# Optimization experiments

Measured on AMD Instinct MI355X. Metric: run time of the kernel, lower is better.

Reference implementation:

```python
import jax, jax.numpy as jnp
import numpy as np

D_MODEL = 1024
NHEAD = 16
DFF = 4096
EPS = 1e-5


def layer_norm(x, g, b, eps=EPS):
    mu = jnp.mean(x, axis=-1, keepdims=True)
    var = jnp.var(x, axis=-1, keepdims=True)
    return (x - mu) * jax.lax.rsqrt(var + eps) * g + b


def setup_inputs() -> dict:
    key = jax.random.key(0)
    ks = jax.random.split(key, 8)
    S, N, E = 1024, 8, D_MODEL
    s = 0.02
    return {
        "src": jax.random.normal(ks[0], (S, N, E), dtype=jnp.float32),
        "in_proj_w": jax.random.normal(ks[1], (3 * E, E), dtype=jnp.float32) * s,
        "in_proj_b": jnp.zeros((3 * E,), dtype=jnp.float32),
        "out_w": jax.random.normal(ks[2], (E, E), dtype=jnp.float32) * s,
        "out_b": jnp.zeros((E,), dtype=jnp.float32),
        "w1": jax.random.normal(ks[3], (DFF, E), dtype=jnp.float32) * s,
        "b1": jnp.zeros((DFF,), dtype=jnp.float32),
        "w2": jax.random.normal(ks[4], (E, DFF), dtype=jnp.float32) * s,
        "b2": jnp.zeros((E,), dtype=jnp.float32),
        "ln1_g": jnp.ones((E,), dtype=jnp.float32),
        "ln1_b": jnp.zeros((E,), dtype=jnp.float32),
        "ln2_g": jnp.ones((E,), dtype=jnp.float32),
        "ln2_b": jnp.zeros((E,), dtype=jnp.float32),
    }


def reference(src, in_proj_w, in_proj_b, out_w, out_b, w1, b1, w2, b2,
              ln1_g, ln1_b, ln2_g, ln2_b):
    S, N, E = src.shape
    H = NHEAD
    D = E // H
    scale = 1.0 / jnp.sqrt(jnp.asarray(D, src.dtype))

    # fused QKV projection (PyTorch in_proj): [S,N,3E]
    qkv = src @ in_proj_w.T + in_proj_b
    q, k, v = jnp.split(qkv, 3, axis=-1)
    # [S,N,E] -> [N,H,S,D]
    def to_heads(t):
        return t.reshape(S, N, H, D).transpose(1, 2, 0, 3)
    q, k, v = to_heads(q), to_heads(k), to_heads(v)

    # explicit QK^T / softmax / AV (need_weights=True path)
    scores = jnp.einsum('nhsd,nhtd->nhst', q * scale, k)  # [N,H,S,S]
    attn = jax.nn.softmax(scores, axis=-1)
    ctx = jnp.einsum('nhst,nhtd->nhsd', attn, v)          # [N,H,S,D]
    ctx = ctx.transpose(2, 0, 1, 3).reshape(S, N, E)
    attn_out = ctx @ out_w.T + out_b

    # avg over heads (PyTorch default average_attn_weights=True): [N,S,S]
    attn_weights = jnp.mean(attn, axis=1)

    # post-norm residual structure (norm_first=False), dropout=0 (eval)
    x = layer_norm(src + attn_out, ln1_g, ln1_b)
    ff = jax.nn.relu(x @ w1.T + b1) @ w2.T + b2
    x = layer_norm(x + ff, ln2_g, ln2_b)
    return x, attn_weights
```

## Files before the change

kernel.cpp:

```cpp
#include <hip/hip_runtime.h>

typedef __attribute__((ext_vector_type(4))) float f32x4;
typedef __attribute__((ext_vector_type(8))) short short8;
typedef __attribute__((ext_vector_type(4))) unsigned short u16x4;

#define MFMA(a,b,c) __builtin_amdgcn_mfma_f32_16x16x32_bf16(a,b,c,0,0,0)

__device__ __forceinline__ unsigned short f2bf(float x){
    union { float f; unsigned int u; } c; c.f = x;
    unsigned int u = c.u;
    unsigned int r = (u + 0x7fffu + ((u >> 16) & 1u)) >> 16;
    return (unsigned short)r;
}
__device__ __forceinline__ float bf2f(unsigned short h){
    union { unsigned int u; float f; } c; c.u = ((unsigned int)h) << 16;
    return c.f;
}

__device__ __forceinline__ void load16_lds(const unsigned short* g, unsigned short* l){
    __builtin_amdgcn_global_load_lds(
        (const __attribute__((address_space(1))) unsigned int*)g,
        (__attribute__((address_space(3))) unsigned int*)l, 16, 0, 0);
}

#define SWZ_IDX(row, col, stride) \
    ((row)*(stride) + (((((col) >> 3) ^ ((row) & 7)) << 3) | ((col) & 7)))

__global__ __launch_bounds__(256) void cast_f32_bf16(const float* __restrict__ in,
                                                     unsigned short* __restrict__ out, int n4){
    int i = blockIdx.x * 256 + threadIdx.x;
    if (i < n4){
        const float4* in4 = (const float4*)in;
        float4 v = in4[i];
        u16x4 o;
        o[0] = f2bf(v.x); o[1] = f2bf(v.y); o[2] = f2bf(v.z); o[3] = f2bf(v.w);
        ((u16x4*)out)[i] = o;
    }
}

template<int OUT_BF16, int RELU>
__global__ __launch_bounds__(256) void gemm_bt(const unsigned short* __restrict__ A,
                                               const unsigned short* __restrict__ W,
                                               const float* __restrict__ bias,
                                               void* __restrict__ Cout,
                                               int M, int N, int K)
{
    __shared__ unsigned short As[128*32];
    __shared__ unsigned short Bs[128*32];
    const int tid  = threadIdx.x;
    const int wave = tid >> 6, lane = tid & 63;
    const int bm = blockIdx.x, bn = blockIdx.y;
    const int wr = wave >> 1, wc = wave & 1;
    const int lr = lane & 15, lg = lane >> 4;

    f32x4 acc[4][4] = {};

    const size_t arow0 = (size_t)bm * 128;
    const size_t brow0 = (size_t)bn * 128;

    for (int k0 = 0; k0 < K; k0 += 32){
        __syncthreads();
        #pragma unroll
        for (int i = 0; i < 2; ++i){
            int c = i*256 + wave*64 + lane;
            int row = c >> 2, cc = c & 3;
            load16_lds(A + (arow0 + row)*K + k0 + cc*8, As + (size_t)(i*256 + wave*64)*8);
            load16_lds(W + (brow0 + row)*K + k0 + cc*8, Bs + (size_t)(i*256 + wave*64)*8);
        }
        __syncthreads();
        short8 af[4], bfr[4];
        #pragma unroll
        for (int mi = 0; mi < 4; ++mi)
            af[mi] = *(const short8*)(As + (wr*64 + mi*16 + lr)*32 + lg*8);
        #pragma unroll
        for (int ni = 0; ni < 4; ++ni)
            bfr[ni] = *(const short8*)(Bs + (wc*64 + ni*16 + lr)*32 + lg*8);
        #pragma unroll
        for (int mi = 0; mi < 4; ++mi)
            #pragma unroll
            for (int ni = 0; ni < 4; ++ni)
                acc[mi][ni] = MFMA(af[mi], bfr[ni], acc[mi][ni]);
    }

    #pragma unroll
    for (int ni = 0; ni < 4; ++ni){
        int col = bn*128 + wc*64 + ni*16 + lr;
        float bv = bias ? bias[col] : 0.0f;
        #pragma unroll
        for (int mi = 0; mi < 4; ++mi){
            int row0 = bm*128 + wr*64 + mi*16 + lg*4;
            #pragma unroll
            for (int j = 0; j < 4; ++j){
                float v = acc[mi][ni][j] + bv;
                if (RELU) v = v > 0.0f ? v : 0.0f;
                if (OUT_BF16) ((unsigned short*)Cout)[(size_t)(row0+j)*N + col] = f2bf(v);
                else          ((float*)Cout)[(size_t)(row0+j)*N + col] = v;
            }
        }
    }
}

__global__ __launch_bounds__(256) void transpose_v(const unsigned short* __restrict__ qkv,
                                                   unsigned short* __restrict__ vt)
{
    __shared__ unsigned short tile[64][80];
    const int tt = blockIdx.x, h = blockIdx.y, n = blockIdx.z;
    const int tid = threadIdx.x;
    #pragma unroll
    for (int i = 0; i < 2; ++i){
        int c = i*256 + tid;
        int row = c >> 3, cc = c & 7;
        short8 v = *(const short8*)(qkv + ((size_t)(tt*64+row)*8 + n)*3072 + 2048 + h*64 + cc*8);
        *(short8*)&tile[row][cc*8] = v;
    }
    __syncthreads();
    #pragma unroll
    for (int i = 0; i < 2; ++i){
        int c = i*256 + tid;
        int drow = c >> 3, cc = c & 7;
        short8 o;
        #pragma unroll
        for (int j = 0; j < 8; ++j) o[j] = tile[cc*8+j][drow];
        *(short8*)(vt + ((size_t)(n*16+h)*64 + drow)*1024 + tt*64 + cc*8) = o;
    }
}

__global__ __launch_bounds__(256) void attn_fused(const unsigned short* __restrict__ qkv,
                                                  const unsigned short* __restrict__ vt,
                                                  float2* __restrict__ stats,
                                                  unsigned short* __restrict__ ctx)
{
    __shared__ unsigned short qs[32*64];
    __shared__ unsigned short kt[64*64];
    __shared__ unsigned short vtile[64*64];
    __shared__ unsigned short pt[32*64];
    __shared__ float wl[4][32];
    __shared__ float rowinv[32];
    const int qb = blockIdx.x, h = blockIdx.y, n = blockIdx.z;
    const int tid = threadIdx.x;
    const int wave = tid >> 6, lane = tid & 63;
    const int lr = lane & 15, lg = lane >> 4;
    const int s0 = qb * 32;
    const float scale = 0.125f;

    {
        int row = tid >> 3, cc = tid & 7;
        *(short8*)(qs + SWZ_IDX(row, cc*8, 64)) =
            *(const short8*)(qkv + ((size_t)(s0+row)*8 + n)*3072 + h*64 + cc*8);
    }

    float lsum[2][4] = {};
    f32x4 av[2] = {};

    for (int tt = 0; tt < 16; ++tt){
        __syncthreads();
        #pragma unroll
        for (int i = 0; i < 2; ++i){
            int c = i*256 + wave*64 + lane;
            int row = c >> 3, sl = (c & 7) ^ (row & 7);
            load16_lds(qkv + ((size_t)(tt*64+row)*8 + n)*3072 + 1024 + h*64 + sl*8,
                       kt + (size_t)(i*256 + wave*64)*8);
            load16_lds(vt + ((size_t)(n*16+h)*64 + row)*1024 + tt*64 + sl*8,
                       vtile + (size_t)(i*256 + wave*64)*8);
        }
        __syncthreads();

        f32x4 acc[2] = {};
        #pragma unroll
        for (int kk = 0; kk < 2; ++kk){
            short8 b  = *(const short8*)(kt + SWZ_IDX(wave*16 + lr, kk*32 + lg*8, 64));
            short8 a0 = *(const short8*)(qs + SWZ_IDX(lr,          kk*32 + lg*8, 64));
            short8 a1 = *(const short8*)(qs + SWZ_IDX(16 + lr,     kk*32 + lg*8, 64));
            acc[0] = MFMA(a0, b, acc[0]);
            acc[1] = MFMA(a1, b, acc[1]);
        }
        #pragma unroll
        for (int mi = 0; mi < 2; ++mi)
            #pragma unroll
            for (int j = 0; j < 4; ++j){
                float p = __expf(fminf(acc[mi][j] * scale, 80.0f));
                lsum[mi][j] += p;
                pt[SWZ_IDX(mi*16 + lg*4 + j, wave*16 + lr, 64)] = f2bf(p);
            }
        __syncthreads();

        #pragma unroll
        for (int kk = 0; kk < 2; ++kk){
            short8 b  = *(const short8*)(vtile + SWZ_IDX(wave*16 + lr, kk*32 + lg*8, 64));
            short8 a0 = *(const short8*)(pt + SWZ_IDX(lr,      kk*32 + lg*8, 64));
            short8 a1 = *(const short8*)(pt + SWZ_IDX(16 + lr, kk*32 + lg*8, 64));
            av[0] = MFMA(a0, b, av[0]);
            av[1] = MFMA(a1, b, av[1]);
        }
    }

    #pragma unroll
    for (int mi = 0; mi < 2; ++mi)
        #pragma unroll
        for (int j = 0; j < 4; ++j){
            float v = lsum[mi][j];
            v += __shfl_xor(v, 1);
            v += __shfl_xor(v, 2);
            v += __shfl_xor(v, 4);
            v += __shfl_xor(v, 8);
            if (lr == 0) wl[wave][mi*16 + lg*4 + j] = v;
        }
    __syncthreads();
    if (tid < 32){
        float l = wl[0][tid] + wl[1][tid] + wl[2][tid] + wl[3][tid];
        float inv = 1.0f / l;
        rowinv[tid] = inv;
        stats[((size_t)(n*16+h)*1024) + s0 + tid] = make_float2(0.0f, inv * 0.0625f);
    }
    __syncthreads();

    #pragma unroll
    for (int mi = 0; mi < 2; ++mi)
        #pragma unroll
        for (int j = 0; j < 4; ++j){
            int lrow = mi*16 + lg*4 + j;
            int srow = s0 + lrow;
            int d = wave*16 + lr;
            ctx[((size_t)srow*8 + n)*1024 + h*64 + d] = f2bf(av[mi][j] * rowinv[lrow]);
        }
}

__global__ __launch_bounds__(256) void attn_mean(const unsigned short* __restrict__ qkv,
                                                 const float2* __restrict__ stats,
                                                 float* __restrict__ attw)
{
    __shared__ unsigned short qs[16*1024];
    __shared__ unsigned short kv[2][4][16*128];
    __shared__ float2 smL[16][16];
    const int qb = blockIdx.x, n = blockIdx.y;
    const int tid = threadIdx.x;
    const int wave = tid >> 6, lane = tid & 63;
    const int lr = lane & 15, lg = lane >> 4;
    const int s0 = qb * 16;
    const float scale = 0.125f;

    {
        int head = tid >> 4, row = tid & 15;
        smL[head][row] = stats[((size_t)(n*16+head)*1024) + s0 + row];
    }
    #pragma unroll
    for (int i = 0; i < 8; ++i){
        int c = i*256 + tid;
        int row = c >> 7, cc = c & 127;
        *(short8*)(qs + SWZ_IDX(row, cc*8, 1024)) =
            *(const short8*)(qkv + ((size_t)(s0+row)*8 + n)*3072 + cc*8);
    }

    unsigned short* kvw = &kv[0][wave][0];
    const int KVBUF = 4*16*128;

    auto stage = [&](int buf, int tt, int g){
        #pragma unroll
        for (int i = 0; i < 4; ++i){
            int c2 = i*64 + lane;
            int rw = c2 >> 4;
            int sd = c2 & 15;
            int sl = sd ^ (rw & 7);
            int trow = tt*64 + wave*16 + rw;
            load16_lds(qkv + ((size_t)trow*8 + n)*3072 + 1024 + g*128 + sl*8,
                       kvw + buf*KVBUF + i*512);
        }
    };

    __syncthreads();
    stage(0, 0, 0);

    float* obase = attw + (size_t)n*1024*1024;
    int r = 0;
    for (int tt = 0; tt < 16; ++tt){
        f32x4 racc = {0.0f, 0.0f, 0.0f, 0.0f};
        for (int g = 0; g < 8; ++g, ++r){
            int nr = r + 1;
            if (nr < 128) stage(nr & 1, nr >> 3, nr & 7);
            if (r < 127) asm volatile("s_waitcnt vmcnt(4)" ::: "memory");
            else         asm volatile("s_waitcnt vmcnt(0)" ::: "memory");
            const unsigned short* kb = kvw + (r & 1)*KVBUF;
            #pragma unroll
            for (int hh = 0; hh < 2; ++hh){
                f32x4 acc = {0.0f, 0.0f, 0.0f, 0.0f};
                #pragma unroll
                for (int kk = 0; kk < 2; ++kk){
                    short8 b = *(const short8*)(kb + SWZ_IDX(lr, hh*64 + kk*32 + lg*8, 128));
                    short8 a = *(const short8*)(qs + SWZ_IDX(lr, g*128 + hh*64 + kk*32 + lg*8, 1024));
                    acc = MFMA(a, b, acc);
                }
                #pragma unroll
                for (int j = 0; j < 4; ++j){
                    float2 mc = smL[g*2 + hh][lg*4 + j];
                    racc[j] += __expf(fminf(acc[j]*scale, 80.0f) - mc.x) * mc.y;
                }
            }
        }
        #pragma unroll
        for (int j = 0; j < 4; ++j)
            obase[(size_t)(s0 + lg*4 + j)*1024 + tt*64 + wave*16 + lr] = racc[j];
    }
}

__global__ __launch_bounds__(256) void add_ln(const float* __restrict__ a,
                                              const float* __restrict__ b,
                                              const float* __restrict__ g,
                                              const float* __restrict__ be,
                                              float* __restrict__ out32,
                                              unsigned short* __restrict__ outbf)
{
    __shared__ float red[8];
    const int row = blockIdx.x;
    const int tid = threadIdx.x;
    const int wave = tid >> 6, lane = tid & 63;
    float4 va = ((const float4*)(a + (size_t)row*1024))[tid];
    float4 vb = ((const float4*)(b + (size_t)row*1024))[tid];
    float x0 = va.x + vb.x, x1 = va.y + vb.y, x2 = va.z + vb.z, x3 = va.w + vb.w;
    float s  = x0 + x1 + x2 + x3;
    float sq = x0*x0 + x1*x1 + x2*x2 + x3*x3;
    #pragma unroll
    for (int off = 1; off < 64; off <<= 1){
        s  += __shfl_xor(s,  off);
        sq += __shfl_xor(sq, off);
    }
    if (lane == 0){ red[wave] = s; red[4+wave] = sq; }
    __syncthreads();
    s  = red[0] + red[1] + red[2] + red[3];
    sq = red[4] + red[5] + red[6] + red[7];
    float mean = s * (1.0f/1024.0f);
    float var  = sq * (1.0f/1024.0f) - mean*mean;
    float rstd = rsqrtf(var + 1e-5f);
    int c = tid * 4;
    float4 vg = ((const float4*)(g  + c))[0];
    float4 vbeta = ((const float4*)(be + c))[0];
    float y0 = (x0-mean)*rstd*vg.x + vbeta.x;
    float y1 = (x1-mean)*rstd*vg.y + vbeta.y;
    float y2 = (x2-mean)*rstd*vg.z + vbeta.z;
    float y3 = (x3-mean)*rstd*vg.w + vbeta.w;
    float4 o; o.x=y0; o.y=y1; o.z=y2; o.w=y3;
    ((float4*)(out32 + (size_t)row*1024))[tid] = o;
    if (outbf){
        u16x4 ob; ob[0]=f2bf(y0); ob[1]=f2bf(y1); ob[2]=f2bf(y2); ob[3]=f2bf(y3);
        ((u16x4*)(outbf + (size_t)row*1024))[tid] = ob;
    }
}

extern "C" void kernel_launch(void* const* d_in, const int* in_sizes, int n_in,
                              void* d_out, int out_size, void* d_ws, size_t ws_size,
                              hipStream_t stream)
{
    (void)in_sizes; (void)n_in; (void)out_size; (void)ws_size;
    const float* src  = (const float*)d_in[0];
    const float* wqkv = (const float*)d_in[1];
    const float* bqkv = (const float*)d_in[2];
    const float* wout = (const float*)d_in[3];
    const float* bout = (const float*)d_in[4];
    const float* w1   = (const float*)d_in[5];
    const float* b1   = (const float*)d_in[6];
    const float* w2   = (const float*)d_in[7];
    const float* b2   = (const float*)d_in[8];
    const float* g1   = (const float*)d_in[9];
    const float* be1  = (const float*)d_in[10];
    const float* g2   = (const float*)d_in[11];
    const float* be2  = (const float*)d_in[12];

    char* ws = (char*)d_ws;
    const size_t MB = 1ull << 20;
    unsigned short* wqkv_bf = (unsigned short*)(ws + 0*MB);
    unsigned short* wout_bf = (unsigned short*)(ws + 6*MB);
    unsigned short* w1_bf   = (unsigned short*)(ws + 8*MB);
    unsigned short* w2_bf   = (unsigned short*)(ws + 16*MB);
    unsigned short* src_bf  = (unsigned short*)(ws + 24*MB);
    unsigned short* x1_bf   = (unsigned short*)(ws + 24*MB);
    unsigned short* qkv_bf  = (unsigned short*)(ws + 40*MB);
    unsigned short* vt_bf   = (unsigned short*)(ws + 88*MB);
    unsigned short* ff1_bf  = (unsigned short*)(ws + 40*MB);
    unsigned short* ctx_bf  = (unsigned short*)(ws + 104*MB);
    float* attn_out = (float*)(ws + 120*MB);
    float* ff2_f32  = (float*)(ws + 120*MB);
    float* x1_f32   = (float*)(ws + 152*MB);
    float2* stats   = (float2*)(ws + 184*MB);

    float* x_out    = (float*)d_out;
    float* attw_out = (float*)d_out + (size_t)8192*1024;

    auto cast = [&](const float* in, unsigned short* out, int nelem){
        int n4 = nelem / 4;
        hipLaunchKernelGGL(cast_f32_bf16, dim3((n4 + 255)/256), dim3(256), 0, stream, in, out, n4);
    };
    cast(wqkv, wqkv_bf, 3072*1024);
    cast(wout, wout_bf, 1024*1024);
    cast(w1,   w1_bf,   4096*1024);
    cast(w2,   w2_bf,   1024*4096);
    cast(src,  src_bf,  8192*1024);

    hipLaunchKernelGGL((gemm_bt<1,0>), dim3(64,24), dim3(256), 0, stream,
                       src_bf, wqkv_bf, bqkv, (void*)qkv_bf, 8192, 3072, 1024);
    hipLaunchKernelGGL(transpose_v, dim3(16,16,8), dim3(256), 0, stream, qkv_bf, vt_bf);
    hipLaunchKernelGGL(attn_fused, dim3(32,16,8), dim3(256), 0, stream,
                       qkv_bf, vt_bf, stats, ctx_bf);
    hipLaunchKernelGGL(attn_mean, dim3(64,8), dim3(256), 0, stream,
                       qkv_bf, stats, attw_out);
    hipLaunchKernelGGL((gemm_bt<0,0>), dim3(64,8), dim3(256), 0, stream,
                       ctx_bf, wout_bf, bout, (void*)attn_out, 8192, 1024, 1024);
    hipLaunchKernelGGL(add_ln, dim3(8192), dim3(256), 0, stream,
                       src, attn_out, g1, be1, x1_f32, x1_bf);
    hipLaunchKernelGGL((gemm_bt<1,1>), dim3(64,32), dim3(256), 0, stream,
                       x1_bf, w1_bf, b1, (void*)ff1_bf, 8192, 4096, 1024);
    hipLaunchKernelGGL((gemm_bt<0,0>), dim3(64,8), dim3(256), 0, stream,
                       ff1_bf, w2_bf, b2, (void*)ff2_f32, 8192, 1024, 4096);
    hipLaunchKernelGGL(add_ln, dim3(8192), dim3(256), 0, stream,
                       x1_f32, ff2_f32, g2, be2, x_out, nullptr);
}
```

Baseline: 578.9 us.

## Double-buffer per-wave private LDS tiles in GEMM to drop block barriers

The bf16 GEMM now gives each wave its own LDS region holding the A and W rows it needs. Loads are double-buffered and ordered with s_waitcnt vmcnt instead of __syncthreads, so the next K-slice streams in while the current one feeds MFMAs. The cost is redundant global traffic, since waves sharing rows each load them, and LDS use grows to 64KB, which may lower occupancy. Relying only on vmcnt without an LDS-visibility wait, and with no barrier before a buffer is overwritten, may be fragile.

```diff
diff --git a/kernel.cpp b/kernel.cpp
--- a/kernel.cpp
+++ b/kernel.cpp
@@ -45,8 +45,7 @@
                                                void* __restrict__ Cout,
                                                int M, int N, int K)
 {
-    __shared__ unsigned short As[128*32];
-    __shared__ unsigned short Bs[128*32];
+    __shared__ unsigned short sh[2][4][4096];
     const int tid  = threadIdx.x;
     const int wave = tid >> 6, lane = tid & 63;
     const int bm = blockIdx.x, bn = blockIdx.y;
@@ -55,26 +54,43 @@
 
     f32x4 acc[4][4] = {};
 
-    const size_t arow0 = (size_t)bm * 128;
-    const size_t brow0 = (size_t)bn * 128;
-
-    for (int k0 = 0; k0 < K; k0 += 32){
-        __syncthreads();
-        #pragma unroll
-        for (int i = 0; i < 2; ++i){
-            int c = i*256 + wave*64 + lane;
-            int row = c >> 2, cc = c & 3;
-            load16_lds(A + (arow0 + row)*K + k0 + cc*8, As + (size_t)(i*256 + wave*64)*8);
-            load16_lds(W + (brow0 + row)*K + k0 + cc*8, Bs + (size_t)(i*256 + wave*64)*8);
-        }
-        __syncthreads();
+    const unsigned short* Abase = A + ((size_t)bm*128 + wr*64) * K;
+    const unsigned short* Wbase = W + ((size_t)bn*128 + wc*64) * K;
+
+    auto stage = [&](int buf, int k0){
+        unsigned short* dst = &sh[buf][wave][0];
+        #pragma unroll
+        for (int i = 0; i < 4; ++i){
+            int c = i*64 + lane;
+            int row = c >> 2, sl = c & 3;
+            load16_lds(Abase + (size_t)row*K + k0 + sl*8, dst + c*8);
+        }
+        #pragma unroll
+        for (int i = 0; i < 4; ++i){
+            int c = i*64 + lane;
+            int row = c >> 2, sl = c & 3;
+            load16_lds(Wbase + (size_t)row*K + k0 + sl*8, dst + 4096/2 + c*8);
+        }
+    };
+
+    stage(0, 0);
+    int it = 0;
+    for (int k0 = 0; k0 < K; k0 += 32, ++it){
+        if (k0 + 32 < K){
+            stage((it+1)&1, k0+32);
+            asm volatile("s_waitcnt vmcnt(8)" ::: "memory");
+        } else {
+            asm volatile("s_waitcnt vmcnt(0)" ::: "memory");
+        }
+        const unsigned short* Ra = &sh[it&1][wave][0];
+        const unsigned short* Rb = Ra + 2048;
         short8 af[4], bfr[4];
         #pragma unroll
         for (int mi = 0; mi < 4; ++mi)
-            af[mi] = *(const short8*)(As + (wr*64 + mi*16 + lr)*32 + lg*8);
+            af[mi] = *(const short8*)(Ra + (mi*16 + lr)*32 + lg*8);
         #pragma unroll
         for (int ni = 0; ni < 4; ++ni)
-            bfr[ni] = *(const short8*)(Bs + (wc*64 + ni*16 + lr)*32 + lg*8);
+            bfr[ni] = *(const short8*)(Rb + (ni*16 + lr)*32 + lg*8);
         #pragma unroll
         for (int mi = 0; mi < 4; ++mi)
             #pragma unroll
```

Result: slower. 602.7 us (+4.1%).

## Add 256x256 tiled GEMM with swizzled double-buffered LDS for QKV and FFN1

Applied to the files above, without the earlier changes.

Adds a new GEMM kernel with 256x256 output tiles, 512 threads and K-step 64. It double-buffers LDS with async global-to-LDS loads and an XOR swizzle to avoid bank conflicts, and raises wave priority around the MFMA block. The QKV projection and FFN1 GEMMs now use it. The goal is more data reuse per tile and overlapping loads with MFMA. The cost is 128KB of LDS and many accumulator registers, and the large tiles leave few blocks (384 and 512) for the CU count.

```diff
diff --git a/kernel.cpp b/kernel.cpp
--- a/kernel.cpp
+++ b/kernel.cpp
@@ -89,6 +89,94 @@
         #pragma unroll
         for (int mi = 0; mi < 4; ++mi){
             int row0 = bm*128 + wr*64 + mi*16 + lg*4;
+            #pragma unroll
+            for (int j = 0; j < 4; ++j){
+                float v = acc[mi][ni][j] + bv;
+                if (RELU) v = v > 0.0f ? v : 0.0f;
+                if (OUT_BF16) ((unsigned short*)Cout)[(size_t)(row0+j)*N + col] = f2bf(v);
+                else          ((float*)Cout)[(size_t)(row0+j)*N + col] = v;
+            }
+        }
+    }
+}
+
+template<int OUT_BF16, int RELU>
+__global__ __launch_bounds__(512) void gemm256(const unsigned short* __restrict__ A,
+                                               const unsigned short* __restrict__ W,
+                                               const float* __restrict__ bias,
+                                               void* __restrict__ Cout,
+                                               int M, int N, int K)
+{
+    __shared__ unsigned short Asw[2][256*64];
+    __shared__ unsigned short Bsw[2][256*64];
+    const int tid  = threadIdx.x;
+    const int wave = tid >> 6, lane = tid & 63;
+    const int wr = wave >> 2, wc = wave & 3;
+    const int lr = lane & 15, lg = lane >> 4;
+    const int bm = blockIdx.x, bn = blockIdx.y;
+
+    f32x4 acc[8][4] = {};
+
+    const unsigned short* Ab = A + (size_t)bm*256*K;
+    const unsigned short* Wb = W + (size_t)bn*256*K;
+
+    auto stage = [&](int buf, int k0){
+        #pragma unroll
+        for (int i = 0; i < 4; ++i){
+            int c = i*512 + tid;
+            int row = c >> 3, sl = (c & 7) ^ (row & 7);
+            load16_lds(Ab + (size_t)row*K + k0 + sl*8, &Asw[buf][0] + (size_t)c*8);
+        }
+        #pragma unroll
+        for (int i = 0; i < 4; ++i){
+            int c = i*512 + tid;
+            int row = c >> 3, sl = (c & 7) ^ (row & 7);
+            load16_lds(Wb + (size_t)row*K + k0 + sl*8, &Bsw[buf][0] + (size_t)c*8);
+        }
+    };
+
+    stage(0, 0);
+    const int NT = K >> 6;
+    for (int t = 0; t < NT; ++t){
+        const int cur = t & 1;
+        if (t + 1 < NT){
+            stage(cur ^ 1, (t+1) << 6);
+            asm volatile("s_waitcnt vmcnt(8)" ::: "memory");
+        } else {
+            asm volatile("s_waitcnt vmcnt(0)" ::: "memory");
+        }
+        __builtin_amdgcn_s_barrier();
+        asm volatile("" ::: "memory");
+        const unsigned short* Al = &Asw[cur][0];
+        const unsigned short* Bl = &Bsw[cur][0];
+        #pragma unroll
+        for (int kk = 0; kk < 2; ++kk){
+            short8 af[8], bf[4];
+            #pragma unroll
+            for (int mi = 0; mi < 8; ++mi)
+                af[mi] = *(const short8*)(Al + SWZ_IDX(wr*128 + mi*16 + lr, kk*32 + lg*8, 64));
+            #pragma unroll
+            for (int ni = 0; ni < 4; ++ni)
+                bf[ni] = *(const short8*)(Bl + SWZ_IDX(wc*64 + ni*16 + lr, kk*32 + lg*8, 64));
+            __builtin_amdgcn_s_setprio(1);
+            #pragma unroll
+            for (int mi = 0; mi < 8; ++mi)
+                #pragma unroll
+                for (int ni = 0; ni < 4; ++ni)
+                    acc[mi][ni] = MFMA(af[mi], bf[ni], acc[mi][ni]);
+            __builtin_amdgcn_s_setprio(0);
+        }
+        asm volatile("" ::: "memory");
+        __builtin_amdgcn_s_barrier();
+    }
+
+    #pragma unroll
+    for (int ni = 0; ni < 4; ++ni){
+        int col = bn*256 + wc*64 + ni*16 + lr;
+        float bv = bias ? bias[col] : 0.0f;
+        #pragma unroll
+        for (int mi = 0; mi < 8; ++mi){
+            int row0 = bm*256 + wr*128 + mi*16 + lg*4;
             #pragma unroll
             for (int j = 0; j < 4; ++j){
                 float v = acc[mi][ni][j] + bv;
@@ -394,7 +482,7 @@
     cast(w2,   w2_bf,   1024*4096);
     cast(src,  src_bf,  8192*1024);
 
-    hipLaunchKernelGGL((gemm_bt<1,0>), dim3(64,24), dim3(256), 0, stream,
+    hipLaunchKernelGGL((gemm256<1,0>), dim3(32,12), dim3(512), 0, stream,
                        src_bf, wqkv_bf, bqkv, (void*)qkv_bf, 8192, 3072, 1024);
     hipLaunchKernelGGL(transpose_v, dim3(16,16,8), dim3(256), 0, stream, qkv_bf, vt_bf);
     hipLaunchKernelGGL(attn_fused, dim3(32,16,8), dim3(256), 0, stream,
@@ -405,7 +493,7 @@
                        ctx_bf, wout_bf, bout, (void*)attn_out, 8192, 1024, 1024);
     hipLaunchKernelGGL(add_ln, dim3(8192), dim3(256), 0, stream,
                        src, attn_out, g1, be1, x1_f32, x1_bf);
-    hipLaunchKernelGGL((gemm_bt<1,1>), dim3(64,32), dim3(256), 0, stream,
+    hipLaunchKernelGGL((gemm256<1,1>), dim3(32,16), dim3(512), 0, stream,
                        x1_bf, w1_bf, b1, (void*)ff1_bf, 8192, 4096, 1024);
     hipLaunchKernelGGL((gemm_bt<0,0>), dim3(64,8), dim3(256), 0, stream,
                        ff1_bf, w2_bf, b2, (void*)ff2_f32, 8192, 1024, 4096);
```

Measured after the change: 559.2 us. -3.4%, faster.
